# Optimization experiments

Measured on AMD Instinct MI355X. Metric: run time of the kernel, lower is better.

## Reference

```python
import jax, jax.numpy as jnp
import numpy as np

B, K, T, H, D = 16, 49, 256, 512, 512


def setup_inputs() -> dict:
    key = jax.random.key(0)
    ks = jax.random.split(key, 8)
    s = 1.0 / np.sqrt(H)
    return {
        "V": jax.random.normal(ks[0], (B, K, H), jnp.float32),
        "h_t": jax.random.normal(ks[1], (B, T, H), jnp.float32),
        "s_t": jax.random.normal(ks[2], (B, T, H), jnp.float32),
        "Wv": jax.random.normal(ks[3], (H, D), jnp.float32) * s,
        "bv": jnp.zeros((D,), jnp.float32),
        "Wg": jax.random.normal(ks[4], (H, D), jnp.float32) * s,
        "bg": jnp.zeros((D,), jnp.float32),
        "Ws": jax.random.normal(ks[5], (H, D), jnp.float32) * s,
        "bs": jnp.zeros((D,), jnp.float32),
        "Wh": jax.random.normal(ks[6], (D, 1), jnp.float32) * (1.0 / np.sqrt(D)),
        "bh": jnp.zeros((1,), jnp.float32),
    }


def reference(V, h_t, s_t, Wv, bv, Wg, bg, Ws, bs, Wh, bh):
    # projections (dropout is identity in eval)
    cv = V @ Wv + bv                        # [B, K, D]
    cg = h_t @ Wg + bg                      # [B, T, D]
    # content_v: [B, T, K, D] via broadcast add
    content_v = cv[:, None, :, :] + cg[:, :, None, :]
    z_t = (jnp.tanh(content_v) @ Wh + bh)[..., 0]   # [B, T, K]
    alpha_t = jax.nn.softmax(z_t, axis=-1)          # [B, T, K]
    c_t = jnp.einsum('btk,bkh->bth', alpha_t, V)    # [B, T, H]
    # sentinel branch
    content_s = (s_t @ Ws + bs) + cg                # [B, T, D]
    z_ext = jnp.tanh(content_s) @ Wh + bh           # [B, T, 1]
    extended = jnp.concatenate([z_t, z_ext], axis=-1)  # [B, T, K+1]
    alpha_hat = jax.nn.softmax(extended, axis=-1)
    beta_t = alpha_hat[:, :, -1:]                   # [B, T, 1]
    c_hat_t = beta_t * s_t + (1.0 - beta_t) * c_t   # [B, T, H]
    return (c_hat_t, alpha_t, beta_t)
```

## Files before the change

kernel.cpp:

```cpp
#include <hip/hip_runtime.h>
#include <hip/hip_fp16.h>
#include <cstdint>
#include <cstddef>

#define B_ 16
#define K_ 49
#define T_ 256
#define H_ 512
#define D_ 512

#define TANH_SCALE 2.8853900817779268f
#define LOG2E 1.4426950408889634f

typedef _Float16 half8 __attribute__((ext_vector_type(8)));
typedef float floatx4 __attribute__((ext_vector_type(4)));

#define ROWS_A 9088
#define OFF_V 0
#define OFF_H 896
#define OFF_S 4992

__device__ __forceinline__ void async16(const _Float16* g, const _Float16* l) {
    __builtin_amdgcn_global_load_lds(
        (const __attribute__((address_space(1))) unsigned int*)g,
        (__attribute__((address_space(3))) unsigned int*)l, 16, 0, 0);
}

__global__ __launch_bounds__(256) void conv_all(const float* __restrict__ V,
                                                const float* __restrict__ h_t,
                                                const float* __restrict__ s_t,
                                                const float* __restrict__ Wv,
                                                const float* __restrict__ Wg,
                                                const float* __restrict__ Ws,
                                                _Float16* __restrict__ Af16,
                                                _Float16* __restrict__ Wt) {
    __shared__ float tile[32][33];
    int tid = threadIdx.x;
    if (blockIdx.x < 2272) {
        int idx = (blockIdx.x * 256 + tid) * 8;
        int row = idx >> 9;
        int col = idx & 511;
        const float* src;
        if (row < 784)        src = V   + (size_t)row * 512 + col;
        else if (row < 896)   src = nullptr;
        else if (row < 4992)  src = h_t + (size_t)(row - 896) * 512 + col;
        else                  src = s_t + (size_t)(row - 4992) * 512 + col;
        half8 h;
        if (src) {
            float4 f0 = *(const float4*)(src);
            float4 f1 = *(const float4*)(src + 4);
            h[0] = (_Float16)f0.x; h[1] = (_Float16)f0.y;
            h[2] = (_Float16)f0.z; h[3] = (_Float16)f0.w;
            h[4] = (_Float16)f1.x; h[5] = (_Float16)f1.y;
            h[6] = (_Float16)f1.z; h[7] = (_Float16)f1.w;
        } else {
            h = (half8)((_Float16)0.0f);
        }
        *(half8*)(Af16 + idx) = h;
    } else {
        int bid = blockIdx.x - 2272;
        int p = bid >> 8;
        int rem = bid & 255;
        int bx = rem & 15, by = rem >> 4;
        const float* W = (p == 0) ? Wv : (p == 1) ? Wg : Ws;
        _Float16* outp = Wt + (size_t)p * 512 * 512;
        int tx = tid & 31, ty = tid >> 5;
        int c = bx * 32 + tx;
        int rbase = by * 32;
#pragma unroll
        for (int i = 0; i < 4; i++)
            tile[ty + i * 8][tx] = W[(size_t)(rbase + ty + i * 8) * 512 + c];
        __syncthreads();
        int k = rbase + tx;
#pragma unroll
        for (int i = 0; i < 4; i++) {
            int n = bx * 32 + ty + i * 8;
            outp[(size_t)n * 512 + k] = (_Float16)(tile[tx][ty + i * 8] * TANH_SCALE);
        }
    }
}

__global__ __launch_bounds__(256) void gemm_f16(
    const _Float16* __restrict__ Af16, const _Float16* __restrict__ Wt,
    const float* __restrict__ bv, const float* __restrict__ bg2,
    const float* __restrict__ bs, float* __restrict__ cv,
    float* __restrict__ cg, float* __restrict__ cs) {
    __shared__ __align__(16) _Float16 As[3][64 * 64];
    __shared__ __align__(16) _Float16 Bs[3][64 * 64];

    int bid = blockIdx.x;
    int id = (bid & 7) * 142 + (bid >> 3);

    int rowbase; const _Float16* Bt; const float* bias; float* C;
    if (id < 112)       { rowbase = OFF_V;            Bt = Wt;          bias = bv;  C = cv; }
    else if (id < 624)  { id -= 112; rowbase = OFF_H; Bt = Wt + 262144; bias = bg2; C = cg; }
    else                { id -= 624; rowbase = OFF_S; Bt = Wt + 524288; bias = bs;  C = cs; }
    int tm = id >> 3, tn = id & 7;

    int tid = threadIdx.x;
    int wave = tid >> 6, lane = tid & 63;

    const _Float16* gA[2]; int ldsOff[2];
    const _Float16* gB[2];
#pragma unroll
    for (int i = 0; i < 2; i++) {
        int p = i * 256 + tid;
        int ks = p >> 8, x = (p >> 6) & 3, q = (p >> 4) & 3, f = p & 15;
        gA[i] = Af16 + (size_t)(rowbase + tm * 64 + x * 16 + f) * 512 + ks * 32 + q * 8;
        gB[i] = Bt   + (size_t)(tn * 64 + x * 16 + f) * 512 + ks * 32 + q * 8;
        ldsOff[i] = p * 8;
    }

    floatx4 acc[4];
#pragma unroll
    for (int x = 0; x < 4; x++) acc[x] = (floatx4)0.0f;

#pragma unroll
    for (int i = 0; i < 2; i++) async16(gA[i], &As[0][ldsOff[i]]);
#pragma unroll
    for (int i = 0; i < 2; i++) async16(gB[i], &Bs[0][ldsOff[i]]);
#pragma unroll
    for (int i = 0; i < 2; i++) async16(gA[i] + 64, &As[1][ldsOff[i]]);
#pragma unroll
    for (int i = 0; i < 2; i++) async16(gB[i] + 64, &Bs[1][ldsOff[i]]);

#pragma unroll
    for (int kk = 0; kk < 8; kk++) {
        const int cur = kk % 3;
        if (kk < 7) {
            asm volatile("s_waitcnt vmcnt(4)" ::: "memory");
        } else {
            asm volatile("s_waitcnt vmcnt(0)" ::: "memory");
        }
        __builtin_amdgcn_s_barrier();
        __builtin_amdgcn_sched_barrier(0);

        if (kk < 6) {
            const int nb = (kk + 2) % 3;
#pragma unroll
            for (int i = 0; i < 2; i++) async16(gA[i] + (kk + 2) * 64, &As[nb][ldsOff[i]]);
#pragma unroll
            for (int i = 0; i < 2; i++) async16(gB[i] + (kk + 2) * 64, &Bs[nb][ldsOff[i]]);
        }

#pragma unroll
        for (int ks = 0; ks < 2; ks++) {
            half8 a[4];
#pragma unroll
            for (int x = 0; x < 4; x++)
                a[x] = *(const half8*)&As[cur][(ks * 256 + x * 64 + lane) * 8];
            half8 b = *(const half8*)&Bs[cur][(ks * 256 + wave * 64 + lane) * 8];
#pragma unroll
            for (int x = 0; x < 4; x++)
                acc[x] = __builtin_amdgcn_mfma_f32_16x16x32_f16(a[x], b, acc[x], 0, 0, 0);
        }
    }

    int dn = lane & 15, dq = lane >> 4;
    int colg = tn * 64 + wave * 16 + dn;
    float bc = bias[colg] * TANH_SCALE;
#pragma unroll
    for (int x = 0; x < 4; x++) {
        int rowg = tm * 64 + x * 16 + dq * 4;
#pragma unroll
        for (int r = 0; r < 4; r++)
            C[(size_t)(rowg + r) * 512 + colg] = __builtin_amdgcn_exp2f(acc[x][r] + bc);
    }
}

__device__ __forceinline__ float wave_sum(float v) {
#pragma unroll
    for (int o = 32; o > 0; o >>= 1) v += __shfl_xor(v, o);
    return v;
}
__device__ __forceinline__ float wave_max(float v) {
#pragma unroll
    for (int o = 32; o > 0; o >>= 1) v = fmaxf(v, __shfl_xor(v, o));
    return v;
}

__device__ __forceinline__ float xsum4(float a0, float a1, float a2, float a3, int lane) {
    bool hi = (lane & 32) != 0;
    float t0 = hi ? a0 : a2;
    float t1 = hi ? a1 : a3;
    t0 = __shfl_xor(t0, 32);
    t1 = __shfl_xor(t1, 32);
    if (hi) { a0 = t0; a1 = t1; } else { a2 = t0; a3 = t1; }
    bool h2 = (lane & 16) != 0;
    float u0 = h2 ? a0 : a1;
    float u1 = h2 ? a2 : a3;
    u0 = __shfl_xor(u0, 16);
    u1 = __shfl_xor(u1, 16);
    if (h2) { a0 = u0; a2 = u1; } else { a1 = u0; a3 = u1; }
    float s = (a0 + a1) + (a2 + a3);
#pragma unroll
    for (int o = 8; o > 0; o >>= 1) s += __shfl_xor(s, o);
    return s;
}

#define TB 4
__global__ __launch_bounds__(256) void z_kernel(
    const float* __restrict__ ecv, const float* __restrict__ ecg,
    const float* __restrict__ ecs, const float* __restrict__ V,
    const float* __restrict__ s_t, const float* __restrict__ Wh,
    const float* __restrict__ bh, float* __restrict__ out) {
    int bx = blockIdx.x;
    int b  = bx >> 6;
    int t0 = (bx & 63) << 2;
    int bt0 = b * 256 + t0;
    int tid = threadIdx.x;
    int wave = tid >> 6, lane = tid & 63;

    __shared__ float zl[TB][64];
    __shared__ float4 al4[52];
    __shared__ float bl[TB];

    float whv[8], egv[TB][8];
#pragma unroll
    for (int j = 0; j < 8; j++) whv[j] = Wh[j * 64 + lane];
#pragma unroll
    for (int tt = 0; tt < TB; tt++) {
        const float* cgp = ecg + (size_t)(bt0 + tt) * 512;
#pragma unroll
        for (int j = 0; j < 8; j++) egv[tt][j] = cgp[j * 64 + lane];
    }
    float s8 = 0.0f;
#pragma unroll
    for (int j = 0; j < 8; j++) s8 += whv[j];
    float zbase = wave_sum(s8) + bh[0];

    float rv[8], rn[8];
    {
        const float* rp = ecv + (size_t)(b * 49 + wave) * 512;
#pragma unroll
        for (int j = 0; j < 8; j++) rv[j] = rp[j * 64 + lane];
    }
    for (int task = wave; task < 49; task += 4) {
        int nt = task + 4;
        if (nt < 49) {
            const float* rp = ecv + (size_t)(b * 49 + nt) * 512;
#pragma unroll
            for (int j = 0; j < 8; j++) rn[j] = rp[j * 64 + lane];
        }
        float acc[TB] = {0.0f, 0.0f, 0.0f, 0.0f};
#pragma unroll
        for (int tt = 0; tt < TB; tt++) {
#pragma unroll
            for (int j = 0; j < 8; j++) {
                float t = fmaf(rv[j], egv[tt][j], 1.0f);
                float r = __builtin_amdgcn_rcpf(t);
                acc[tt] = fmaf(whv[j], r, acc[tt]);
            }
        }
        float z = xsum4(acc[0], acc[1], acc[2], acc[3], lane);
        if ((lane & 15) == 0) zl[lane >> 4][task] = zbase - 2.0f * z;
#pragma unroll
        for (int j = 0; j < 8; j++) rv[j] = rn[j];
    }
#pragma unroll
    for (int tt = 0; tt < TB; tt++) {
        if (wave == tt) {
            const float* rp = ecs + (size_t)(bt0 + tt) * 512;
            float acc = 0.0f;
#pragma unroll
            for (int j = 0; j < 8; j++) {
                float t = fmaf(rp[j * 64 + lane], egv[tt][j], 1.0f);
                float r = __builtin_amdgcn_rcpf(t);
                acc = fmaf(whv[j], r, acc);
            }
            float s = wave_sum(acc);
            if (lane == 0) zl[tt][49] = zbase - 2.0f * s;
        }
    }
    __syncthreads();

    {
        int w = wave;
        float z = (lane < 49) ? zl[w][lane] : -3.0e38f;
        float m = wave_max(z);
        float e = (lane < 49) ? __builtin_amdgcn_exp2f((z - m) * LOG2E) : 0.0f;
        float s = wave_sum(e);
        float zext = zl[w][49];
        float m2 = fmaxf(m, zext);
        float sc   = __builtin_amdgcn_exp2f((m - m2) * LOG2E);
        float eext = __builtin_amdgcn_exp2f((zext - m2) * LOG2E);
        float s2 = s * sc + eext;
        float beta = eext / s2;
        if (lane < 49) {
            float a = e / s;
            ((float*)&al4[lane])[w] = a;
            out[(size_t)B_ * T_ * H_ + (size_t)(bt0 + w) * 49 + lane] = a;
        }
        if (lane == 0) {
            bl[w] = beta;
            out[(size_t)B_ * T_ * H_ + (size_t)B_ * T_ * K_ + (bt0 + w)] = beta;
        }
    }
    __syncthreads();

    const float* Vb = V + (size_t)b * 49 * 512;
    float2 accA[TB];
#pragma unroll
    for (int tt = 0; tt < TB; tt++) accA[tt] = make_float2(0.0f, 0.0f);
#pragma unroll 7
    for (int k = 0; k < 49; k++) {
        float4 a4 = al4[k];
        float2 v = *(const float2*)(Vb + (size_t)k * 512 + tid * 2);
        accA[0].x = fmaf(a4.x, v.x, accA[0].x);  accA[0].y = fmaf(a4.x, v.y, accA[0].y);
        accA[1].x = fmaf(a4.y, v.x, accA[1].x);  accA[1].y = fmaf(a4.y, v.y, accA[1].y);
        accA[2].x = fmaf(a4.z, v.x, accA[2].x);  accA[2].y = fmaf(a4.z, v.y, accA[2].y);
        accA[3].x = fmaf(a4.w, v.x, accA[3].x);  accA[3].y = fmaf(a4.w, v.y, accA[3].y);
    }
#pragma unroll
    for (int tt = 0; tt < TB; tt++) {
        float beta = bl[tt];
        float2 sp = *(const float2*)(s_t + (size_t)(bt0 + tt) * 512 + tid * 2);
        float2 o;
        o.x = beta * sp.x + (1.0f - beta) * accA[tt].x;
        o.y = beta * sp.y + (1.0f - beta) * accA[tt].y;
        *(float2*)(out + (size_t)(bt0 + tt) * 512 + tid * 2) = o;
    }
}

extern "C" void kernel_launch(void* const* d_in, const int* in_sizes, int n_in,
                              void* d_out, int out_size, void* d_ws, size_t ws_size,
                              hipStream_t stream) {
    const float* V   = (const float*)d_in[0];
    const float* h_t = (const float*)d_in[1];
    const float* s_t = (const float*)d_in[2];
    const float* Wv  = (const float*)d_in[3];
    const float* bv  = (const float*)d_in[4];
    const float* bg  = (const float*)d_in[6];
    const float* Ws  = (const float*)d_in[7];
    const float* bs  = (const float*)d_in[8];
    const float* Wg  = (const float*)d_in[5];
    const float* Wh  = (const float*)d_in[9];
    const float* bh  = (const float*)d_in[10];
    float* out = (float*)d_out;

    char* ws = (char*)d_ws;
    _Float16* Af16 = (_Float16*)(ws);
    _Float16* Wt   = (_Float16*)(ws + 9306112);
    float* ecv = (float*)(ws + 10878976);
    float* ecg = (float*)(ws + 12713984);
    float* ecs = (float*)(ws + 21102592);

    conv_all<<<3040, 256, 0, stream>>>(V, h_t, s_t, Wv, Wg, Ws, Af16, Wt);
    gemm_f16<<<1136, 256, 0, stream>>>(Af16, Wt, bv, bg, bs, ecv, ecg, ecs);
    z_kernel<<<1024, 256, 0, stream>>>(ecv, ecg, ecs, V, s_t, Wh, bh, out);
}
```

Measured before the change: 133.9 us.

## Enlarge GEMM tiles to 128x128 with 2x2 wave grid and 4x4 MFMA per wave

The fused projection GEMM moves from 64x64 output tiles (1136 blocks, each wave owning one 16-column strip) to 128x128 tiles (284 blocks, each wave computing a 64x64 sub-tile with 16 accumulators). The K step shrinks to 32 so that LDS per stage stays the same, and the XCD-aware block remapping is adjusted for the new block count. The aim is more MFMA work per LDS fragment load and less redundant global traffic. The cost is higher register pressure and only 284 blocks, fewer than two per CU on a 256-CU part, with possible tail imbalance.

```diff
diff --git a/kernel.cpp b/kernel.cpp
--- a/kernel.cpp
+++ b/kernel.cpp
@@ -85,49 +85,54 @@
     const float* __restrict__ bv, const float* __restrict__ bg2,
     const float* __restrict__ bs, float* __restrict__ cv,
     float* __restrict__ cg, float* __restrict__ cs) {
-    __shared__ __align__(16) _Float16 As[3][64 * 64];
-    __shared__ __align__(16) _Float16 Bs[3][64 * 64];
+    __shared__ __align__(16) _Float16 As[3][128 * 32];
+    __shared__ __align__(16) _Float16 Bs[3][128 * 32];
 
     int bid = blockIdx.x;
-    int id = (bid & 7) * 142 + (bid >> 3);
+    int jj = bid >> 3, xcd = bid & 7;
+    int id = (xcd < 4) ? xcd * 36 + jj : 144 + (xcd - 4) * 35 + jj;
 
     int rowbase; const _Float16* Bt; const float* bias; float* C;
-    if (id < 112)       { rowbase = OFF_V;            Bt = Wt;          bias = bv;  C = cv; }
-    else if (id < 624)  { id -= 112; rowbase = OFF_H; Bt = Wt + 262144; bias = bg2; C = cg; }
-    else                { id -= 624; rowbase = OFF_S; Bt = Wt + 524288; bias = bs;  C = cs; }
-    int tm = id >> 3, tn = id & 7;
+    if (id < 28)        {            rowbase = OFF_V; Bt = Wt;          bias = bv;  C = cv; }
+    else if (id < 156)  { id -= 28;  rowbase = OFF_H; Bt = Wt + 262144; bias = bg2; C = cg; }
+    else                { id -= 156; rowbase = OFF_S; Bt = Wt + 524288; bias = bs;  C = cs; }
+    int mrel = (id >> 2) * 128;
+    int m0 = rowbase + mrel;
+    int n0 = (id & 3) * 128;
 
     int tid = threadIdx.x;
     int wave = tid >> 6, lane = tid & 63;
-
-    const _Float16* gA[2]; int ldsOff[2];
-    const _Float16* gB[2];
+    int wr = wave >> 1, wc = wave & 1;
+
+    const _Float16* gA[2]; const _Float16* gB[2]; int ldsOff[2];
 #pragma unroll
     for (int i = 0; i < 2; i++) {
-        int p = i * 256 + tid;
-        int ks = p >> 8, x = (p >> 6) & 3, q = (p >> 4) & 3, f = p & 15;
-        gA[i] = Af16 + (size_t)(rowbase + tm * 64 + x * 16 + f) * 512 + ks * 32 + q * 8;
-        gB[i] = Bt   + (size_t)(tn * 64 + x * 16 + f) * 512 + ks * 32 + q * 8;
-        ldsOff[i] = p * 8;
-    }
-
-    floatx4 acc[4];
-#pragma unroll
-    for (int x = 0; x < 4; x++) acc[x] = (floatx4)0.0f;
+        int c = i * 256 + tid;
+        int x8 = c >> 6, q = (c >> 4) & 3, f = c & 15;
+        gA[i] = Af16 + (size_t)(m0 + x8 * 16 + f) * 512 + q * 8;
+        gB[i] = Bt   + (size_t)(n0 + x8 * 16 + f) * 512 + q * 8;
+        ldsOff[i] = c * 8;
+    }
+
+    floatx4 acc[4][4];
+#pragma unroll
+    for (int x = 0; x < 4; x++)
+#pragma unroll
+        for (int y = 0; y < 4; y++) acc[x][y] = (floatx4)0.0f;
 
 #pragma unroll
     for (int i = 0; i < 2; i++) async16(gA[i], &As[0][ldsOff[i]]);
 #pragma unroll
     for (int i = 0; i < 2; i++) async16(gB[i], &Bs[0][ldsOff[i]]);
 #pragma unroll
-    for (int i = 0; i < 2; i++) async16(gA[i] + 64, &As[1][ldsOff[i]]);
-#pragma unroll
-    for (int i = 0; i < 2; i++) async16(gB[i] + 64, &Bs[1][ldsOff[i]]);
-
-#pragma unroll
-    for (int kk = 0; kk < 8; kk++) {
+    for (int i = 0; i < 2; i++) async16(gA[i] + 32, &As[1][ldsOff[i]]);
+#pragma unroll
+    for (int i = 0; i < 2; i++) async16(gB[i] + 32, &Bs[1][ldsOff[i]]);
+
+#pragma unroll
+    for (int kk = 0; kk < 16; kk++) {
         const int cur = kk % 3;
-        if (kk < 7) {
+        if (kk < 15) {
             asm volatile("s_waitcnt vmcnt(4)" ::: "memory");
         } else {
             asm volatile("s_waitcnt vmcnt(0)" ::: "memory");
@@ -135,36 +140,39 @@
         __builtin_amdgcn_s_barrier();
         __builtin_amdgcn_sched_barrier(0);
 
-        if (kk < 6) {
+        if (kk < 14) {
             const int nb = (kk + 2) % 3;
 #pragma unroll
-            for (int i = 0; i < 2; i++) async16(gA[i] + (kk + 2) * 64, &As[nb][ldsOff[i]]);
-#pragma unroll
-            for (int i = 0; i < 2; i++) async16(gB[i] + (kk + 2) * 64, &Bs[nb][ldsOff[i]]);
-        }
-
-#pragma unroll
-        for (int ks = 0; ks < 2; ks++) {
-            half8 a[4];
-#pragma unroll
-            for (int x = 0; x < 4; x++)
-                a[x] = *(const half8*)&As[cur][(ks * 256 + x * 64 + lane) * 8];
-            half8 b = *(const half8*)&Bs[cur][(ks * 256 + wave * 64 + lane) * 8];
-#pragma unroll
-            for (int x = 0; x < 4; x++)
-                acc[x] = __builtin_amdgcn_mfma_f32_16x16x32_f16(a[x], b, acc[x], 0, 0, 0);
-        }
+            for (int i = 0; i < 2; i++) async16(gA[i] + (kk + 2) * 32, &As[nb][ldsOff[i]]);
+#pragma unroll
+            for (int i = 0; i < 2; i++) async16(gB[i] + (kk + 2) * 32, &Bs[nb][ldsOff[i]]);
+        }
+
+        half8 a[4], b[4];
+#pragma unroll
+        for (int t = 0; t < 4; t++) {
+            a[t] = *(const half8*)&As[cur][((wr * 4 + t) * 64 + lane) * 8];
+            b[t] = *(const half8*)&Bs[cur][((wc * 4 + t) * 64 + lane) * 8];
+        }
+#pragma unroll
+        for (int x = 0; x < 4; x++)
+#pragma unroll
+            for (int y = 0; y < 4; y++)
+                acc[x][y] = __builtin_amdgcn_mfma_f32_16x16x32_f16(a[x], b[y], acc[x][y], 0, 0, 0);
     }
 
     int dn = lane & 15, dq = lane >> 4;
-    int colg = tn * 64 + wave * 16 + dn;
-    float bc = bias[colg] * TANH_SCALE;
-#pragma unroll
-    for (int x = 0; x < 4; x++) {
-        int rowg = tm * 64 + x * 16 + dq * 4;
-#pragma unroll
-        for (int r = 0; r < 4; r++)
-            C[(size_t)(rowg + r) * 512 + colg] = __builtin_amdgcn_exp2f(acc[x][r] + bc);
+#pragma unroll
+    for (int y = 0; y < 4; y++) {
+        int colg = n0 + wc * 64 + y * 16 + dn;
+        float bc = bias[colg] * TANH_SCALE;
+#pragma unroll
+        for (int x = 0; x < 4; x++) {
+            int rowg = mrel + wr * 64 + x * 16 + dq * 4;
+#pragma unroll
+            for (int r = 0; r < 4; r++)
+                C[(size_t)(rowg + r) * 512 + colg] = __builtin_amdgcn_exp2f(acc[x][y][r] + bc);
+        }
     }
 }
 
@@ -330,10 +338,10 @@
     const float* s_t = (const float*)d_in[2];
     const float* Wv  = (const float*)d_in[3];
     const float* bv  = (const float*)d_in[4];
+    const float* Wg  = (const float*)d_in[5];
     const float* bg  = (const float*)d_in[6];
     const float* Ws  = (const float*)d_in[7];
     const float* bs  = (const float*)d_in[8];
-    const float* Wg  = (const float*)d_in[5];
     const float* Wh  = (const float*)d_in[9];
     const float* bh  = (const float*)d_in[10];
     float* out = (float*)d_out;
@@ -346,6 +354,6 @@
     float* ecs = (float*)(ws + 21102592);
 
     conv_all<<<3040, 256, 0, stream>>>(V, h_t, s_t, Wv, Wg, Ws, Af16, Wt);
-    gemm_f16<<<1136, 256, 0, stream>>>(Af16, Wt, bv, bg, bs, ecv, ecg, ecs);
+    gemm_f16<<<284, 256, 0, stream>>>(Af16, Wt, bv, bg, bs, ecv, ecg, ecs);
     z_kernel<<<1024, 256, 0, stream>>>(ecv, ecg, ecs, V, s_t, Wh, bh, out);
 }
```

Result: no change. 132.6 us (-1.0%).
